# Kernel tuning notes

Hardware: AMD Instinct MI355X
Metric: run time of the kernel (lower is better)

## Reference

```python
import jax, jax.numpy as jnp
import numpy as np

N_NODES = 20000
N_EDGES = 640000
K_CHEB = 20


def setup_inputs() -> dict:
    key = jax.random.key(0)
    ks = jax.random.split(key, 8)
    x = jax.random.normal(ks[0], (128, N_NODES, 1), dtype=jnp.float32)
    rows = jax.random.randint(ks[1], (N_EDGES,), 0, N_NODES, dtype=jnp.int32)
    cols = jax.random.randint(ks[2], (N_EDGES,), 0, N_NODES, dtype=jnp.int32)
    # rescaled-Laplacian-like values, small scale so the K=20 recursion stays bounded
    vals = jax.random.normal(ks[3], (N_EDGES,), dtype=jnp.float32) * 0.05
    W_gc = jax.random.normal(ks[4], (K_CHEB, 10), dtype=jnp.float32) * 0.1
    b_gc = jnp.zeros((10,), dtype=jnp.float32)
    W_fc = jax.random.normal(ks[5], (N_NODES * 10, 10), dtype=jnp.float32) * 0.01
    b_fc = jnp.zeros((10,), dtype=jnp.float32)
    return {"x": x, "rows": rows, "cols": cols, "vals": vals,
            "W_gc": W_gc, "b_gc": b_gc, "W_fc": W_fc, "b_fc": b_fc}


def reference(x, rows, cols, vals, W_gc, b_gc, W_fc, b_fc):
    B, N, Fin = x.shape  # Fin == 1
    x0 = x[..., 0].T  # [N, B]

    def spmm(t):  # sparse L @ t via edge-list scatter-add, t: [N, B]
        return jax.ops.segment_sum(vals[:, None] * t[cols], rows, num_segments=N)

    # Chebyshev recursion: T0 = x, T1 = L x, Tk = 2 L T_{k-1} - T_{k-2}
    Ts = [x0, spmm(x0)]
    for _ in range(K_CHEB - 2):
        Ts.append(2.0 * spmm(Ts[-1]) - Ts[-2])
    Xt = jnp.stack(Ts, axis=-1)  # [N, B, K]

    gc = jnp.einsum('nbk,kf->bnf', Xt, W_gc) + b_gc  # [B, N, 10]
    gc = jax.nn.relu(gc)
    flat = gc.reshape(B, N * 10)
    h = jax.nn.relu(flat @ W_fc + b_fc)  # [B, 10]
    return jax.nn.softmax(h, axis=1)
```

## Files before the change

kernel.cpp:

```cpp
#include <hip/hip_runtime.h>
#include <hip/hip_bf16.h>
#include <hip/hip_fp16.h>
#include <math.h>


#define NF 10
#define KCHEB 20
#define BCG 64
#define COFF16 (KCHEB * BCG)

typedef unsigned int u32;


__global__ void init_kernel(int* counts, float* h_part, const float* __restrict__ W_gc,
                            float* __restrict__ WgT, int N, int H) {
    int i = blockIdx.x * blockDim.x + threadIdx.x;
    if (i < N) counts[i] = 0;
    if (i < H) h_part[i] = 0.f;
    if (i < KCHEB * NF) WgT[(i % NF) * KCHEB + (i / NF)] = W_gc[i];
}

__global__ void hist_kernel(const int* __restrict__ rows, int* __restrict__ counts, int E) {
    int e = blockIdx.x * blockDim.x + threadIdx.x;
    if (e < E) atomicAdd(&counts[rows[e]], 1);
}

#define SB 1024
__global__ void scan1_kernel(const int* __restrict__ counts, int* __restrict__ ex,
                             int* __restrict__ bsum, int N) {
    __shared__ int sh[SB];
    int t = threadIdx.x;
    int i = blockIdx.x * SB + t;
    int v = (i < N) ? counts[i] : 0;
    sh[t] = v;
    __syncthreads();
    for (int off = 1; off < SB; off <<= 1) {
        int u = (t >= off) ? sh[t - off] : 0;
        __syncthreads();
        sh[t] += u;
        __syncthreads();
    }
    if (i < N) ex[i] = sh[t] - v;
    if (t == SB - 1) bsum[blockIdx.x] = sh[t];
}

__global__ void scan2_kernel(const int* __restrict__ bsum, int* __restrict__ boff, int nb) {
    if (threadIdx.x == 0) {
        int run = 0;
        for (int i = 0; i < nb; ++i) { boff[i] = run; run += bsum[i]; }
        boff[nb] = run;
    }
}

__global__ void scan3_kernel(int* __restrict__ row_start, int* __restrict__ cursor,
                             const int* __restrict__ ex, const int* __restrict__ boff,
                             int N, int nb) {
    int i = blockIdx.x * blockDim.x + threadIdx.x;
    if (i < N) {
        int v = ex[i] + boff[i >> 10];
        row_start[i] = v;
        cursor[i] = v;
    }
    if (i == N) row_start[N] = boff[nb];
}

__global__ void scatter_kernel(const int* __restrict__ rows, const int* __restrict__ cols,
                               const float* __restrict__ vals, int* __restrict__ cursor,
                               int2* __restrict__ csr, int E) {
    int e = blockIdx.x * blockDim.x + threadIdx.x;
    if (e >= E) return;
    int p = atomicAdd(&cursor[rows[e]], 1);
    csr[p] = make_int2(cols[e] * COFF16, __float_as_int(vals[e]));
}


__global__ void transpose_kernel(const float* __restrict__ x, __half* __restrict__ X16,
                                 float* __restrict__ C32, int N, int ntiles, int b0s) {
    __shared__ float tile[BCG][65];
    int tid = threadIdx.x;
    int g = blockIdx.x / ntiles;
    int ti = blockIdx.x - g * ntiles;
    int n0 = ti * 64;
#pragma unroll
    for (int p = 0; p < 16; ++p) {
        int idx = p * 256 + tid;
        int row = idx >> 6;
        int col = idx & 63;
        if (n0 + col < N)
            tile[row][col] = x[(size_t)(b0s + g * BCG + row) * N + n0 + col];
    }
    __syncthreads();
#pragma unroll
    for (int p = 0; p < 16; ++p) {
        int idx = p * 256 + tid;
        int nloc = idx >> 6;
        int bb = idx & 63;
        int n = n0 + nloc;
        if (n < N) {
            float v = tile[bb][nloc];
            X16[(size_t)(g * N + n) * COFF16 + bb] = __float2half_rn(v);
            C32[((size_t)(g * 2 + 0) * N + n) * BCG + bb] = v;
        }
    }
}


__global__ __launch_bounds__(256)
void spmm_kernel(__half* __restrict__ X16, float* __restrict__ C32,
                 const int* __restrict__ row_start, const int2* __restrict__ csr,
                 int N, int xpcShift, int subsPerChunk,
                 int kIn, int kOut, float alpha, float beta) {
    int xcd = blockIdx.x & 7;
    int chunk = xcd >> xpcShift;
    int xpcMask = (1 << xpcShift) - 1;
    int sub = (blockIdx.x >> 3) * (1 << xpcShift) + (xcd & xpcMask);
    if (sub >= subsPerChunk) return;
    int tid = threadIdx.x;
    int ln = tid >> 3;
    int bq = tid & 7;
    int n = sub * 32 + ln;
    if (n >= N) return;
    int s = row_start[n];
    int e = row_start[n + 1];

    const __half* gin = X16 + (size_t)chunk * N * COFF16;
    int koff = kIn * BCG + bq * 8;
    int bo = bq * 8;
    float acc[8];
#pragma unroll
    for (int q = 0; q < 8; ++q) acc[q] = 0.f;

    int i = s;
    for (; i + 4 <= e; i += 4) {
        int2 p0 = csr[i], p1 = csr[i + 1], p2 = csr[i + 2], p3 = csr[i + 3];
        uint4 u0 = *(const uint4*)(gin + p0.x + koff);
        uint4 u1 = *(const uint4*)(gin + p1.x + koff);
        uint4 u2 = *(const uint4*)(gin + p2.x + koff);
        uint4 u3 = *(const uint4*)(gin + p3.x + koff);
        float v0 = __int_as_float(p0.y), v1 = __int_as_float(p1.y);
        float v2 = __int_as_float(p2.y), v3 = __int_as_float(p3.y);
        {
            float2 f0 = __half22float2(*(__half2*)&u0.x), f1 = __half22float2(*(__half2*)&u0.y);
            float2 f2 = __half22float2(*(__half2*)&u0.z), f3 = __half22float2(*(__half2*)&u0.w);
            acc[0] += v0 * f0.x; acc[1] += v0 * f0.y; acc[2] += v0 * f1.x; acc[3] += v0 * f1.y;
            acc[4] += v0 * f2.x; acc[5] += v0 * f2.y; acc[6] += v0 * f3.x; acc[7] += v0 * f3.y;
        }
        {
            float2 f0 = __half22float2(*(__half2*)&u1.x), f1 = __half22float2(*(__half2*)&u1.y);
            float2 f2 = __half22float2(*(__half2*)&u1.z), f3 = __half22float2(*(__half2*)&u1.w);
            acc[0] += v1 * f0.x; acc[1] += v1 * f0.y; acc[2] += v1 * f1.x; acc[3] += v1 * f1.y;
            acc[4] += v1 * f2.x; acc[5] += v1 * f2.y; acc[6] += v1 * f3.x; acc[7] += v1 * f3.y;
        }
        {
            float2 f0 = __half22float2(*(__half2*)&u2.x), f1 = __half22float2(*(__half2*)&u2.y);
            float2 f2 = __half22float2(*(__half2*)&u2.z), f3 = __half22float2(*(__half2*)&u2.w);
            acc[0] += v2 * f0.x; acc[1] += v2 * f0.y; acc[2] += v2 * f1.x; acc[3] += v2 * f1.y;
            acc[4] += v2 * f2.x; acc[5] += v2 * f2.y; acc[6] += v2 * f3.x; acc[7] += v2 * f3.y;
        }
        {
            float2 f0 = __half22float2(*(__half2*)&u3.x), f1 = __half22float2(*(__half2*)&u3.y);
            float2 f2 = __half22float2(*(__half2*)&u3.z), f3 = __half22float2(*(__half2*)&u3.w);
            acc[0] += v3 * f0.x; acc[1] += v3 * f0.y; acc[2] += v3 * f1.x; acc[3] += v3 * f1.y;
            acc[4] += v3 * f2.x; acc[5] += v3 * f2.y; acc[6] += v3 * f3.x; acc[7] += v3 * f3.y;
        }
    }
    for (; i < e; ++i) {
        int2 p0 = csr[i];
        uint4 u0 = *(const uint4*)(gin + p0.x + koff);
        float v0 = __int_as_float(p0.y);
        float2 f0 = __half22float2(*(__half2*)&u0.x), f1 = __half22float2(*(__half2*)&u0.y);
        float2 f2 = __half22float2(*(__half2*)&u0.z), f3 = __half22float2(*(__half2*)&u0.w);
        acc[0] += v0 * f0.x; acc[1] += v0 * f0.y; acc[2] += v0 * f1.x; acc[3] += v0 * f1.y;
        acc[4] += v0 * f2.x; acc[5] += v0 * f2.y; acc[6] += v0 * f3.x; acc[7] += v0 * f3.y;
    }

    float* cslot = C32 + ((size_t)(chunk * 2 + (kOut & 1)) * N + n) * BCG + bo;
    float o[8];
#pragma unroll
    for (int q = 0; q < 8; ++q) o[q] = alpha * acc[q];
    if (beta != 0.f) {
        const float4 pv0 = *(const float4*)(cslot);
        const float4 pv1 = *(const float4*)(cslot + 4);
        o[0] += beta * pv0.x; o[1] += beta * pv0.y; o[2] += beta * pv0.z; o[3] += beta * pv0.w;
        o[4] += beta * pv1.x; o[5] += beta * pv1.y; o[6] += beta * pv1.z; o[7] += beta * pv1.w;
    }
    *(float4*)(cslot)     = make_float4(o[0], o[1], o[2], o[3]);
    *(float4*)(cslot + 4) = make_float4(o[4], o[5], o[6], o[7]);
    __half* o16 = X16 + (size_t)(chunk * N + n) * COFF16 + kOut * BCG + bo;
    uint4 h4;
    __half2 h01 = __floats2half2_rn(o[0], o[1]);
    __half2 h23 = __floats2half2_rn(o[2], o[3]);
    __half2 h45 = __floats2half2_rn(o[4], o[5]);
    __half2 h67 = __floats2half2_rn(o[6], o[7]);
    h4.x = *(u32*)&h01; h4.y = *(u32*)&h23; h4.z = *(u32*)&h45; h4.w = *(u32*)&h67;
    *(uint4*)o16 = h4;
}


__global__ __launch_bounds__(1024, 8)
void proj_fc_kernel(const __half* __restrict__ X16,
                    const float* __restrict__ WgT,
                    const float* __restrict__ b_gc,
                    const float* __restrict__ W_fc,
                    float* __restrict__ h_part,
                    int N, int b0s, int G) {
    __shared__ float sRed[BCG * 11];
    int tid = threadIdx.x;
    for (int i = tid; i < BCG * 11; i += 1024) sRed[i] = 0.f;
    __syncthreads();

    int g = blockIdx.x % G;
    int bidx = blockIdx.x / G;
    int nblk = gridDim.x / G;

    int bb = tid & (BCG - 1);
    int wv = __builtin_amdgcn_readfirstlane(tid >> 6);

    float h_loc[NF];
#pragma unroll
    for (int f = 0; f < NF; ++f) h_loc[f] = 0.f;

    const __half* chunkBase = X16 + (size_t)g * N * COFF16;
    int ngroups = (N + 15) / 16;
    for (int grp = bidx; grp < ngroups; grp += nblk) {
        int n = grp * 16 + wv;
        if (n < N) {
            float xt[KCHEB];
            const __half* xp = chunkBase + (size_t)n * COFF16 + bb;
#pragma unroll
            for (int k = 0; k < KCHEB; ++k) xt[k] = __half2float(xp[k * BCG]);

            const float* wfBase = W_fc + (size_t)n * (NF * NF);
#pragma unroll 1
            for (int j = 0; j < NF; ++j) {
                const float* wg = WgT + j * KCHEB;
                float gc = b_gc[j];
#pragma unroll
                for (int k = 0; k < KCHEB; ++k) gc += wg[k] * xt[k];
                gc = fmaxf(gc, 0.f);
                const float* wf = wfBase + j * NF;
#pragma unroll
                for (int f = 0; f < NF; ++f) h_loc[f] += gc * wf[f];
            }
        }
    }
#pragma unroll
    for (int f = 0; f < NF; ++f) atomicAdd(&sRed[bb * 11 + f], h_loc[f]);
    __syncthreads();
    for (int i = tid; i < BCG * NF; i += 1024) {
        int rb = i / NF;
        int rf = i - rb * NF;
        atomicAdd(&h_part[(size_t)(b0s + g * BCG + rb) * NF + rf], sRed[rb * 11 + rf]);
    }
}


__global__ void softmax_kernel(const float* __restrict__ h_part, const float* __restrict__ b_fc,
                               float* __restrict__ out, int B) {
    int b = blockIdx.x * blockDim.x + threadIdx.x;
    if (b >= B) return;
    float v[NF];
    float m = -1e30f;
#pragma unroll
    for (int f = 0; f < NF; ++f) {
        float t = fmaxf(h_part[b * NF + f] + b_fc[f], 0.f);
        v[f] = t;
        m = fmaxf(m, t);
    }
    float s = 0.f;
#pragma unroll
    for (int f = 0; f < NF; ++f) { v[f] = expf(v[f] - m); s += v[f]; }
    float inv = 1.f / s;
#pragma unroll
    for (int f = 0; f < NF; ++f) out[b * NF + f] = v[f] * inv;
}


extern "C" void kernel_launch(void* const* d_in, const int* in_sizes, int n_in,
                              void* d_out, int out_size, void* d_ws, size_t ws_size,
                              hipStream_t stream) {
    const float* x    = (const float*)d_in[0];
    const int*   rows = (const int*)d_in[1];
    const int*   cols = (const int*)d_in[2];
    const float* vals = (const float*)d_in[3];
    const float* W_gc = (const float*)d_in[4];
    const float* b_gc = (const float*)d_in[5];
    const float* W_fc = (const float*)d_in[6];
    const float* b_fc = (const float*)d_in[7];
    float* out = (float*)d_out;

    const int E = in_sizes[1];
    const int N = in_sizes[6] / (NF * NF);
    const int B = in_sizes[0] / N;

    char* p = (char*)d_ws;
    int* counts    = (int*)p;   p += sizeof(int) * (size_t)N;
    int* row_start = (int*)p;   p += sizeof(int) * (size_t)(N + 1);
    int* cursor    = (int*)p;   p += sizeof(int) * (size_t)N;
    int* exbuf     = (int*)p;   p += sizeof(int) * (size_t)N;
    int* bsum      = (int*)p;   p += sizeof(int) * 64;
    int* boff      = (int*)p;   p += sizeof(int) * 64;
    p = (char*)(((size_t)p + 15) & ~(size_t)15);
    int2* csr      = (int2*)p;  p += sizeof(int2) * (size_t)E;
    float* h_part  = (float*)p; p += sizeof(float) * (size_t)B * NF;
    p = (char*)(((size_t)p + 15) & ~(size_t)15);
    float* WgT     = (float*)p; p += sizeof(float) * (size_t)(NF * KCHEB);
    size_t fixed = (size_t)(p - (char*)d_ws);
    fixed = (fixed + 255) & ~(size_t)255;

    size_t perChunk16 = (size_t)N * COFF16 * sizeof(__half);
    size_t perCarry   = (size_t)2 * N * BCG * sizeof(float);
    int G = (B >= 2 * BCG) ? 2 : 1;
    while (G > 1 && fixed + (size_t)G * (perChunk16 + perCarry) > ws_size) G >>= 1;
    __half* X16 = (__half*)((char*)d_ws + fixed);
    size_t x16b = ((size_t)G * perChunk16 + 255) & ~(size_t)255;
    float* C32 = (float*)((char*)d_ws + fixed + x16b);
    int xpcShift = (G == 2) ? 2 : 3;
    int BT = G * BCG;
    int nsc = B / BT;

    {
        int H = B * NF;
        int cov = (N > H) ? N : H;
        int nb = (N + SB - 1) / SB;
        init_kernel<<<(cov + 255) / 256, 256, 0, stream>>>(counts, h_part, W_gc, WgT, N, H);
        hist_kernel<<<(E + 255) / 256, 256, 0, stream>>>(rows, counts, E);
        scan1_kernel<<<nb, SB, 0, stream>>>(counts, exbuf, bsum, N);
        scan2_kernel<<<1, 64, 0, stream>>>(bsum, boff, nb);
        scan3_kernel<<<(N + 256) / 256, 256, 0, stream>>>(row_start, cursor, exbuf, boff, N, nb);
        scatter_kernel<<<(E + 255) / 256, 256, 0, stream>>>(rows, cols, vals, cursor, csr, E);
    }

    int ntiles = (N + 63) / 64;
    int subsPerChunk = (N + 31) / 32;
    int xpc = 1 << xpcShift;
    int gridSpmm = 8 * ((subsPerChunk + xpc - 1) / xpc);

    for (int c = 0; c < nsc; ++c) {
        int b0s = c * BT;
        transpose_kernel<<<G * ntiles, 256, 0, stream>>>(x, X16, C32, N, ntiles, b0s);
        for (int k = 1; k < KCHEB; ++k) {
            float alpha = (k == 1) ? 1.f : 2.f;
            float beta  = (k == 1) ? 0.f : -1.f;
            spmm_kernel<<<gridSpmm, 256, 0, stream>>>(
                X16, C32, row_start, csr, N, xpcShift, subsPerChunk,
                k - 1, k, alpha, beta);
        }
        proj_fc_kernel<<<256 * G, 1024, 0, stream>>>(X16, WgT, b_gc, W_fc, h_part, N, b0s, G);
    }

    softmax_kernel<<<1, 128, 0, stream>>>(h_part, b_fc, out, B);
}
```

Before: 563.6 us.

## Partition CSR by column block so SpMM gathers sweep column ranges in phases

Builds the CSR keyed by (column block, row), splitting the column range into four quarters so each row has four sub-segments. The SpMM kernel walks the four column blocks one after another, so at any moment the concurrently running waves tend to gather from a smaller slice of the fp16 Chebyshev buffer, which is meant to improve L2/cache hit rates on the random gathers. In exchange, each row does four row_start lookups and four shorter loops with more remainder iterations, and the setup histogram, scan and scatter run over four times as many bins.

```diff
diff --git a/kernel.cpp b/kernel.cpp
--- a/kernel.cpp
+++ b/kernel.cpp
@@ -8,30 +8,35 @@
 #define KCHEB 20
 #define BCG 64
 #define COFF16 (KCHEB * BCG)
+#define NCB 4
 
 typedef unsigned int u32;
 
 
 __global__ void init_kernel(int* counts, float* h_part, const float* __restrict__ W_gc,
-                            float* __restrict__ WgT, int N, int H) {
+                            float* __restrict__ WgT, int NV, int H) {
     int i = blockIdx.x * blockDim.x + threadIdx.x;
-    if (i < N) counts[i] = 0;
+    if (i < NV) counts[i] = 0;
     if (i < H) h_part[i] = 0.f;
     if (i < KCHEB * NF) WgT[(i % NF) * KCHEB + (i / NF)] = W_gc[i];
 }
 
-__global__ void hist_kernel(const int* __restrict__ rows, int* __restrict__ counts, int E) {
+__global__ void hist_kernel(const int* __restrict__ rows, const int* __restrict__ cols,
+                            int* __restrict__ counts, int E, int N, int QS) {
     int e = blockIdx.x * blockDim.x + threadIdx.x;
-    if (e < E) atomicAdd(&counts[rows[e]], 1);
+    if (e < E) {
+        int cb = cols[e] / QS;
+        atomicAdd(&counts[cb * N + rows[e]], 1);
+    }
 }
 
 #define SB 1024
 __global__ void scan1_kernel(const int* __restrict__ counts, int* __restrict__ ex,
-                             int* __restrict__ bsum, int N) {
+                             int* __restrict__ bsum, int NV) {
     __shared__ int sh[SB];
     int t = threadIdx.x;
     int i = blockIdx.x * SB + t;
-    int v = (i < N) ? counts[i] : 0;
+    int v = (i < NV) ? counts[i] : 0;
     sh[t] = v;
     __syncthreads();
     for (int off = 1; off < SB; off <<= 1) {
@@ -40,7 +45,7 @@
         sh[t] += u;
         __syncthreads();
     }
-    if (i < N) ex[i] = sh[t] - v;
+    if (i < NV) ex[i] = sh[t] - v;
     if (t == SB - 1) bsum[blockIdx.x] = sh[t];
 }
 
@@ -54,23 +59,25 @@
 
 __global__ void scan3_kernel(int* __restrict__ row_start, int* __restrict__ cursor,
                              const int* __restrict__ ex, const int* __restrict__ boff,
-                             int N, int nb) {
+                             int NV, int nb) {
     int i = blockIdx.x * blockDim.x + threadIdx.x;
-    if (i < N) {
+    if (i < NV) {
         int v = ex[i] + boff[i >> 10];
         row_start[i] = v;
         cursor[i] = v;
     }
-    if (i == N) row_start[N] = boff[nb];
+    if (i == NV) row_start[NV] = boff[nb];
 }
 
 __global__ void scatter_kernel(const int* __restrict__ rows, const int* __restrict__ cols,
                                const float* __restrict__ vals, int* __restrict__ cursor,
-                               int2* __restrict__ csr, int E) {
+                               int2* __restrict__ csr, int E, int N, int QS) {
     int e = blockIdx.x * blockDim.x + threadIdx.x;
     if (e >= E) return;
-    int p = atomicAdd(&cursor[rows[e]], 1);
-    csr[p] = make_int2(cols[e] * COFF16, __float_as_int(vals[e]));
+    int col = cols[e];
+    int cb = col / QS;
+    int p = atomicAdd(&cursor[cb * N + rows[e]], 1);
+    csr[p] = make_int2(col * COFF16, __float_as_int(vals[e]));
 }
 
 
@@ -120,8 +127,6 @@
     int bq = tid & 7;
     int n = sub * 32 + ln;
     if (n >= N) return;
-    int s = row_start[n];
-    int e = row_start[n + 1];
 
     const __half* gin = X16 + (size_t)chunk * N * COFF16;
     int koff = kIn * BCG + bq * 8;
@@ -130,48 +135,54 @@
 #pragma unroll
     for (int q = 0; q < 8; ++q) acc[q] = 0.f;
 
-    int i = s;
-    for (; i + 4 <= e; i += 4) {
-        int2 p0 = csr[i], p1 = csr[i + 1], p2 = csr[i + 2], p3 = csr[i + 3];
-        uint4 u0 = *(const uint4*)(gin + p0.x + koff);
-        uint4 u1 = *(const uint4*)(gin + p1.x + koff);
-        uint4 u2 = *(const uint4*)(gin + p2.x + koff);
-        uint4 u3 = *(const uint4*)(gin + p3.x + koff);
-        float v0 = __int_as_float(p0.y), v1 = __int_as_float(p1.y);
-        float v2 = __int_as_float(p2.y), v3 = __int_as_float(p3.y);
-        {
+#pragma unroll 1
+    for (int cb = 0; cb < NCB; ++cb) {
+        int vr = cb * N + n;
+        int s = row_start[vr];
+        int e = row_start[vr + 1];
+        int i = s;
+        for (; i + 4 <= e; i += 4) {
+            int2 p0 = csr[i], p1 = csr[i + 1], p2 = csr[i + 2], p3 = csr[i + 3];
+            uint4 u0 = *(const uint4*)(gin + p0.x + koff);
+            uint4 u1 = *(const uint4*)(gin + p1.x + koff);
+            uint4 u2 = *(const uint4*)(gin + p2.x + koff);
+            uint4 u3 = *(const uint4*)(gin + p3.x + koff);
+            float v0 = __int_as_float(p0.y), v1 = __int_as_float(p1.y);
+            float v2 = __int_as_float(p2.y), v3 = __int_as_float(p3.y);
+            {
+                float2 f0 = __half22float2(*(__half2*)&u0.x), f1 = __half22float2(*(__half2*)&u0.y);
+                float2 f2 = __half22float2(*(__half2*)&u0.z), f3 = __half22float2(*(__half2*)&u0.w);
+                acc[0] += v0 * f0.x; acc[1] += v0 * f0.y; acc[2] += v0 * f1.x; acc[3] += v0 * f1.y;
+                acc[4] += v0 * f2.x; acc[5] += v0 * f2.y; acc[6] += v0 * f3.x; acc[7] += v0 * f3.y;
+            }
+            {
+                float2 f0 = __half22float2(*(__half2*)&u1.x), f1 = __half22float2(*(__half2*)&u1.y);
+                float2 f2 = __half22float2(*(__half2*)&u1.z), f3 = __half22float2(*(__half2*)&u1.w);
+                acc[0] += v1 * f0.x; acc[1] += v1 * f0.y; acc[2] += v1 * f1.x; acc[3] += v1 * f1.y;
+                acc[4] += v1 * f2.x; acc[5] += v1 * f2.y; acc[6] += v1 * f3.x; acc[7] += v1 * f3.y;
+            }
+            {
+                float2 f0 = __half22float2(*(__half2*)&u2.x), f1 = __half22float2(*(__half2*)&u2.y);
+                float2 f2 = __half22float2(*(__half2*)&u2.z), f3 = __half22float2(*(__half2*)&u2.w);
+                acc[0] += v2 * f0.x; acc[1] += v2 * f0.y; acc[2] += v2 * f1.x; acc[3] += v2 * f1.y;
+                acc[4] += v2 * f2.x; acc[5] += v2 * f2.y; acc[6] += v2 * f3.x; acc[7] += v2 * f3.y;
+            }
+            {
+                float2 f0 = __half22float2(*(__half2*)&u3.x), f1 = __half22float2(*(__half2*)&u3.y);
+                float2 f2 = __half22float2(*(__half2*)&u3.z), f3 = __half22float2(*(__half2*)&u3.w);
+                acc[0] += v3 * f0.x; acc[1] += v3 * f0.y; acc[2] += v3 * f1.x; acc[3] += v3 * f1.y;
+                acc[4] += v3 * f2.x; acc[5] += v3 * f2.y; acc[6] += v3 * f3.x; acc[7] += v3 * f3.y;
+            }
+        }
+        for (; i < e; ++i) {
+            int2 p0 = csr[i];
+            uint4 u0 = *(const uint4*)(gin + p0.x + koff);
+            float v0 = __int_as_float(p0.y);
             float2 f0 = __half22float2(*(__half2*)&u0.x), f1 = __half22float2(*(__half2*)&u0.y);
             float2 f2 = __half22float2(*(__half2*)&u0.z), f3 = __half22float2(*(__half2*)&u0.w);
             acc[0] += v0 * f0.x; acc[1] += v0 * f0.y; acc[2] += v0 * f1.x; acc[3] += v0 * f1.y;
             acc[4] += v0 * f2.x; acc[5] += v0 * f2.y; acc[6] += v0 * f3.x; acc[7] += v0 * f3.y;
         }
-        {
-            float2 f0 = __half22float2(*(__half2*)&u1.x), f1 = __half22float2(*(__half2*)&u1.y);
-            float2 f2 = __half22float2(*(__half2*)&u1.z), f3 = __half22float2(*(__half2*)&u1.w);
-            acc[0] += v1 * f0.x; acc[1] += v1 * f0.y; acc[2] += v1 * f1.x; acc[3] += v1 * f1.y;
-            acc[4] += v1 * f2.x; acc[5] += v1 * f2.y; acc[6] += v1 * f3.x; acc[7] += v1 * f3.y;
-        }
-        {
-            float2 f0 = __half22float2(*(__half2*)&u2.x), f1 = __half22float2(*(__half2*)&u2.y);
-            float2 f2 = __half22float2(*(__half2*)&u2.z), f3 = __half22float2(*(__half2*)&u2.w);
-            acc[0] += v2 * f0.x; acc[1] += v2 * f0.y; acc[2] += v2 * f1.x; acc[3] += v2 * f1.y;
-            acc[4] += v2 * f2.x; acc[5] += v2 * f2.y; acc[6] += v2 * f3.x; acc[7] += v2 * f3.y;
-        }
-        {
-            float2 f0 = __half22float2(*(__half2*)&u3.x), f1 = __half22float2(*(__half2*)&u3.y);
-            float2 f2 = __half22float2(*(__half2*)&u3.z), f3 = __half22float2(*(__half2*)&u3.w);
-            acc[0] += v3 * f0.x; acc[1] += v3 * f0.y; acc[2] += v3 * f1.x; acc[3] += v3 * f1.y;
-            acc[4] += v3 * f2.x; acc[5] += v3 * f2.y; acc[6] += v3 * f3.x; acc[7] += v3 * f3.y;
-        }
-    }
-    for (; i < e; ++i) {
-        int2 p0 = csr[i];
-        uint4 u0 = *(const uint4*)(gin + p0.x + koff);
-        float v0 = __int_as_float(p0.y);
-        float2 f0 = __half22float2(*(__half2*)&u0.x), f1 = __half22float2(*(__half2*)&u0.y);
-        float2 f2 = __half22float2(*(__half2*)&u0.z), f3 = __half22float2(*(__half2*)&u0.w);
-        acc[0] += v0 * f0.x; acc[1] += v0 * f0.y; acc[2] += v0 * f1.x; acc[3] += v0 * f1.y;
-        acc[4] += v0 * f2.x; acc[5] += v0 * f2.y; acc[6] += v0 * f3.x; acc[7] += v0 * f3.y;
     }
 
     float* cslot = C32 + ((size_t)(chunk * 2 + (kOut & 1)) * N + n) * BCG + bo;
@@ -292,14 +303,16 @@
     const int E = in_sizes[1];
     const int N = in_sizes[6] / (NF * NF);
     const int B = in_sizes[0] / N;
+    const int NV = NCB * N;
+    const int QS = (N + NCB - 1) / NCB;
 
     char* p = (char*)d_ws;
-    int* counts    = (int*)p;   p += sizeof(int) * (size_t)N;
-    int* row_start = (int*)p;   p += sizeof(int) * (size_t)(N + 1);
-    int* cursor    = (int*)p;   p += sizeof(int) * (size_t)N;
-    int* exbuf     = (int*)p;   p += sizeof(int) * (size_t)N;
-    int* bsum      = (int*)p;   p += sizeof(int) * 64;
-    int* boff      = (int*)p;   p += sizeof(int) * 64;
+    int* counts    = (int*)p;   p += sizeof(int) * (size_t)NV;
+    int* row_start = (int*)p;   p += sizeof(int) * (size_t)(NV + 1);
+    int* cursor    = (int*)p;   p += sizeof(int) * (size_t)NV;
+    int* exbuf     = (int*)p;   p += sizeof(int) * (size_t)NV;
+    int* bsum      = (int*)p;   p += sizeof(int) * 160;
+    int* boff      = (int*)p;   p += sizeof(int) * 160;
     p = (char*)(((size_t)p + 15) & ~(size_t)15);
     int2* csr      = (int2*)p;  p += sizeof(int2) * (size_t)E;
     float* h_part  = (float*)p; p += sizeof(float) * (size_t)B * NF;
@@ -321,14 +334,14 @@
 
     {
         int H = B * NF;
-        int cov = (N > H) ? N : H;
-        int nb = (N + SB - 1) / SB;
-        init_kernel<<<(cov + 255) / 256, 256, 0, stream>>>(counts, h_part, W_gc, WgT, N, H);
-        hist_kernel<<<(E + 255) / 256, 256, 0, stream>>>(rows, counts, E);
-        scan1_kernel<<<nb, SB, 0, stream>>>(counts, exbuf, bsum, N);
+        int cov = (NV > H) ? NV : H;
+        int nb = (NV + SB - 1) / SB;
+        init_kernel<<<(cov + 255) / 256, 256, 0, stream>>>(counts, h_part, W_gc, WgT, NV, H);
+        hist_kernel<<<(E + 255) / 256, 256, 0, stream>>>(rows, cols, counts, E, N, QS);
+        scan1_kernel<<<nb, SB, 0, stream>>>(counts, exbuf, bsum, NV);
         scan2_kernel<<<1, 64, 0, stream>>>(bsum, boff, nb);
-        scan3_kernel<<<(N + 256) / 256, 256, 0, stream>>>(row_start, cursor, exbuf, boff, N, nb);
-        scatter_kernel<<<(E + 255) / 256, 256, 0, stream>>>(rows, cols, vals, cursor, csr, E);
+        scan3_kernel<<<(NV + 256) / 256, 256, 0, stream>>>(row_start, cursor, exbuf, boff, NV, nb);
+        scatter_kernel<<<(E + 255) / 256, 256, 0, stream>>>(rows, cols, vals, cursor, csr, E, N, QS);
     }
 
     int ntiles = (N + 63) / 64;
```

Measured after the change: 655.9 us. +16.4%, slower.
